# Performance work log

Measured on AMD Instinct MI355X. Metric: run time of the kernel, lower is better.

Reference implementation:

```python
import jax, jax.numpy as jnp
import numpy as np

B, T, C, HS = 16, 2048, 2048, 256  # batch, seq (=BLOCK_SIZE), N_EMBD, head_size


def setup_inputs() -> dict:
    key = jax.random.key(0)
    k0, k1, k2, k3 = jax.random.split(key, 4)
    token_embd = jax.random.normal(k0, (B, T, C), dtype=jnp.float32)
    # nn.Linear(C, HS, bias=False); store as [C, HS] so projection is x @ W
    scale = 1.0 / np.sqrt(C)
    Wk = jax.random.normal(k1, (C, HS), dtype=jnp.float32) * scale
    Wq = jax.random.normal(k2, (C, HS), dtype=jnp.float32) * scale
    Wv = jax.random.normal(k3, (C, HS), dtype=jnp.float32) * scale
    return {"token_embd": token_embd, "Wk": Wk, "Wq": Wq, "Wv": Wv}


def reference(token_embd, Wk, Wq, Wv):
    Bc, Tc, Cc = token_embd.shape
    k = token_embd @ Wk  # [B,T,HS]
    q = token_embd @ Wq  # [B,T,HS]
    v = token_embd @ Wv  # [B,T,HS]
    # NOTE faithful quirks of the source: k @ q^T (not q @ k^T) and
    # MULTIPLY by sqrt(C) where C = N_EMBD.
    weights = jnp.einsum("bih,bjh->bij", k, q) * (Cc ** 0.5)  # [B,T,T]
    # causal mask: tril==0 (upper triangle, j>i) -> -inf
    i = jnp.arange(Tc)[:, None]
    j = jnp.arange(Tc)[None, :]
    weights = jnp.where(j > i, -jnp.inf, weights)
    # softmax over dim=1 (rows / first T axis), as in the source
    weights = jax.nn.softmax(weights, axis=1)
    # dropout p=0.0 / eval mode -> identity
    output = jnp.einsum("bij,bjh->bih", weights, v)  # [B,T,HS]
    return output
```

## Files before the change

### kernel.cpp

```cpp
#include <hip/hip_runtime.h>
#include <math.h>

#define Bn 16
#define Tn 2048
#define Cn 2048
#define HSn 256
#define SCALE 45.254833995939045f
#define NEG_BIG (-1e30f)
#define NT 16
#define NPAIR 136
#define WN 524288

typedef __attribute__((ext_vector_type(8))) short bf16x8;
typedef __attribute__((ext_vector_type(4))) float f32x4;
typedef unsigned short u16;
typedef unsigned int u32;

__device__ __forceinline__ u16 bf16_rn(float f) {
    u32 u = __float_as_uint(f);
    u += 0x7fffu + ((u >> 16) & 1u);
    return (u16)(u >> 16);
}
__device__ __forceinline__ float bf16_rn_f(float f) {
    return __uint_as_float((u32)bf16_rn(f) << 16);
}

#define GLOAD_LDS16(gp, lp)                                                      \
    __builtin_amdgcn_global_load_lds(                                            \
        (const __attribute__((address_space(1))) unsigned int*)(gp),             \
        (__attribute__((address_space(3))) unsigned int*)(lp), 16, 0, 0)

#define WAITV0_LG0  asm volatile("s_waitcnt vmcnt(0) lgkmcnt(0)" ::: "memory")
#define WAITV2_LG0  asm volatile("s_waitcnt vmcnt(2) lgkmcnt(0)" ::: "memory")
#define WAITV32_LG0 asm volatile("s_waitcnt vmcnt(32) lgkmcnt(0)" ::: "memory")
#define WAITLG0     asm volatile("s_waitcnt lgkmcnt(0)" ::: "memory")
#define BARRIER     __builtin_amdgcn_s_barrier()

__global__ __launch_bounds__(256) void split_w_kernel(
    const float* __restrict__ Wk, const float* __restrict__ Wq,
    const float* __restrict__ Wv, u16* __restrict__ Wt)
{
    const int n = threadIdx.x, k = blockIdx.x, mat = blockIdx.y;
    const float* src = (mat == 0) ? Wk : (mat == 1) ? Wq : Wv;
    const float f = src[(long)k * HSn + n];
    const u32 u = __float_as_uint(f);
    const u16 hb = (u16)(u >> 16);
    const float fh = __uint_as_float(u & 0xffff0000u);
    const u16 lb = bf16_rn(f - fh);
    u16* base = Wt + (long)mat * 2 * WN;
    base[(long)n * Cn + k] = hb;
    base[WN + (long)n * Cn + k] = lb;
}

__global__ __launch_bounds__(512, 2) void projm_fused_kernel(
    const float* __restrict__ X, const u16* __restrict__ Wt,
    u16* __restrict__ Khi, u16* __restrict__ Klo,
    u16* __restrict__ Qhi, u16* __restrict__ Qlo, u16* __restrict__ VbfT)
{
    __shared__ u16 Ahi0[4096], Alo0[4096], Ahi1[4096], Alo1[4096];
    __shared__ u16 Bb0[20480], Bb1[20480];

    const int tid = threadIdx.x, l = tid & 63, w = tid >> 6;
    const int wm = w & 3, wn = w >> 2;
    const int m0 = blockIdx.x * 128, n0 = blockIdx.y * 128;

    int xoff[2], aoff[2];
    #pragma unroll
    for (int p = 0; p < 2; ++p) {
        const int idx4 = p * 512 + tid;
        const int row  = idx4 >> 3;
        const int kk4  = (idx4 & 7) * 4;
        xoff[p] = (m0 + row) * Cn + kk4;
        aoff[p] = (row >> 4) * 512 + (((row & 15) | ((kk4 >> 3) << 4)) * 8) + (kk4 & 7);
    }

    int wgoff[5];
    const int lbase = w * 5 * 512;
    #pragma unroll
    for (int j = 0; j < 5; ++j) {
        const int g    = w * 5 + j;
        const int half = g >> 3;
        const int cc   = g & 7;
        const int nrow = n0 + cc * 16 + (l & 15);
        wgoff[j] = half * WN + nrow * Cn + ((l >> 4) << 3);
    }

    f32x4 accK[2][4], accQ[2][4], accV[2][4];
    #pragma unroll
    for (int mt = 0; mt < 2; ++mt)
        #pragma unroll
        for (int nt = 0; nt < 4; ++nt)
            #pragma unroll
            for (int r = 0; r < 4; ++r) {
                accK[mt][nt][r] = 0.f; accQ[mt][nt][r] = 0.f; accV[mt][nt][r] = 0.f;
            }

    float4 xA[2], xB[2];

    auto convert_write = [&](const float4 (&xr)[2], u16* Ah, u16* Al) {
        #pragma unroll
        for (int p = 0; p < 2; ++p) {
            const float xf[4] = {xr[p].x, xr[p].y, xr[p].z, xr[p].w};
            ushort4 h4, l4;
            #pragma unroll
            for (int c = 0; c < 4; ++c) {
                const u32 u = __float_as_uint(xf[c]);
                ((u16*)&h4)[c] = (u16)(u >> 16);
                const float fh = __uint_as_float(u & 0xffff0000u);
                ((u16*)&l4)[c] = bf16_rn(xf[c] - fh);
            }
            *(ushort4*)(Ah + aoff[p]) = h4;
            *(ushort4*)(Al + aoff[p]) = l4;
        }
    };

    auto mfma_all = [&](const u16* Ah, const u16* Al, const u16* Bb) {
        bf16x8 ah[2], al[2];
        #pragma unroll
        for (int mt = 0; mt < 2; ++mt) {
            ah[mt] = *(const bf16x8*)(Ah + (wm * 2 + mt) * 512 + l * 8);
            al[mt] = *(const bf16x8*)(Al + (wm * 2 + mt) * 512 + l * 8);
        }
        {
            bf16x8 bh[4], bl[4];
            #pragma unroll
            for (int nt = 0; nt < 4; ++nt) {
                bh[nt] = *(const bf16x8*)(Bb + (0 * 8 + wn * 4 + nt) * 512 + l * 8);
                bl[nt] = *(const bf16x8*)(Bb + (1 * 8 + wn * 4 + nt) * 512 + l * 8);
            }
            #pragma unroll
            for (int mt = 0; mt < 2; ++mt)
                #pragma unroll
                for (int nt = 0; nt < 4; ++nt) {
                    accK[mt][nt] = __builtin_amdgcn_mfma_f32_16x16x32_bf16(ah[mt], bh[nt], accK[mt][nt], 0, 0, 0);
                    accK[mt][nt] = __builtin_amdgcn_mfma_f32_16x16x32_bf16(ah[mt], bl[nt], accK[mt][nt], 0, 0, 0);
                    accK[mt][nt] = __builtin_amdgcn_mfma_f32_16x16x32_bf16(al[mt], bh[nt], accK[mt][nt], 0, 0, 0);
                }
        }
        {
            bf16x8 bh[4], bl[4];
            #pragma unroll
            for (int nt = 0; nt < 4; ++nt) {
                bh[nt] = *(const bf16x8*)(Bb + (2 * 8 + wn * 4 + nt) * 512 + l * 8);
                bl[nt] = *(const bf16x8*)(Bb + (3 * 8 + wn * 4 + nt) * 512 + l * 8);
            }
            #pragma unroll
            for (int mt = 0; mt < 2; ++mt)
                #pragma unroll
                for (int nt = 0; nt < 4; ++nt) {
                    accQ[mt][nt] = __builtin_amdgcn_mfma_f32_16x16x32_bf16(ah[mt], bh[nt], accQ[mt][nt], 0, 0, 0);
                    accQ[mt][nt] = __builtin_amdgcn_mfma_f32_16x16x32_bf16(ah[mt], bl[nt], accQ[mt][nt], 0, 0, 0);
                    accQ[mt][nt] = __builtin_amdgcn_mfma_f32_16x16x32_bf16(al[mt], bh[nt], accQ[mt][nt], 0, 0, 0);
                }
        }
        {
            bf16x8 bh[4];
            #pragma unroll
            for (int nt = 0; nt < 4; ++nt)
                bh[nt] = *(const bf16x8*)(Bb + (4 * 8 + wn * 4 + nt) * 512 + l * 8);
            #pragma unroll
            for (int mt = 0; mt < 2; ++mt)
                #pragma unroll
                for (int nt = 0; nt < 4; ++nt)
                    accV[mt][nt] = __builtin_amdgcn_mfma_f32_16x16x32_bf16(ah[mt], bh[nt], accV[mt][nt], 0, 0, 0);
        }
    };

    xA[0] = *(const float4*)(X + xoff[0]);
    xA[1] = *(const float4*)(X + xoff[1]);
    #pragma unroll
    for (int j = 0; j < 5; ++j)
        GLOAD_LDS16(Wt + wgoff[j], Bb0 + lbase + j * 512);
    xB[0] = *(const float4*)(X + xoff[0] + 32);
    xB[1] = *(const float4*)(X + xoff[1] + 32);
    convert_write(xA, Ahi0, Alo0);
    WAITV2_LG0;
    BARRIER;

    #pragma unroll 1
    for (int k0 = 0; k0 < Cn; k0 += 64) {
        const int kn  = (k0 + 64 < Cn) ? k0 + 64 : 0;
        const int kn3 = (k0 + 96 < Cn) ? k0 + 96 : 0;
        #pragma unroll
        for (int j = 0; j < 5; ++j)
            GLOAD_LDS16(Wt + wgoff[j] + k0 + 32, Bb1 + lbase + j * 512);
        xA[0] = *(const float4*)(X + xoff[0] + kn);
        xA[1] = *(const float4*)(X + xoff[1] + kn);
        convert_write(xB, Ahi1, Alo1);
        mfma_all(Ahi0, Alo0, Bb0);
        WAITV2_LG0;
        BARRIER;
        #pragma unroll
        for (int j = 0; j < 5; ++j)
            GLOAD_LDS16(Wt + wgoff[j] + kn, Bb0 + lbase + j * 512);
        xB[0] = *(const float4*)(X + xoff[0] + kn3);
        xB[1] = *(const float4*)(X + xoff[1] + kn3);
        convert_write(xA, Ahi0, Alo0);
        mfma_all(Ahi1, Alo1, Bb1);
        WAITV2_LG0;
        BARRIER;
    }

    const int quad = (l >> 4) * 4, col = l & 15;
    u16* Vlds = Bb0;
    __syncthreads();
    #pragma unroll
    for (int mt = 0; mt < 2; ++mt)
        #pragma unroll
        for (int nt = 0; nt < 4; ++nt)
            #pragma unroll
            for (int r = 0; r < 4; ++r) {
                const long i = m0 + wm * 32 + mt * 16 + quad + r;
                const int  j = n0 + wn * 64 + nt * 16 + col;
                {
                    const float f = accK[mt][nt][r];
                    const u32 u = __float_as_uint(f);
                    Khi[i * HSn + j] = (u16)(u >> 16);
                    const float fh = __uint_as_float(u & 0xffff0000u);
                    Klo[i * HSn + j] = bf16_rn(f - fh);
                }
                {
                    const float f = accQ[mt][nt][r];
                    const u32 u = __float_as_uint(f);
                    Qhi[i * HSn + j] = (u16)(u >> 16);
                    const float fh = __uint_as_float(u & 0xffff0000u);
                    Qlo[i * HSn + j] = bf16_rn(f - fh);
                }
                Vlds[(wm * 32 + mt * 16 + quad + r) * 128 + wn * 64 + nt * 16 + col]
                    = bf16_rn(accV[mt][nt][r]);
            }
    __syncthreads();
    {
        const int bidx = m0 >> 11, jb = m0 & (Tn - 1);
        #pragma unroll
        for (int hh = 0; hh < 4; ++hh) {
            const int hl = hh * 32 + (tid >> 4);
            const int h  = n0 + hl;
            const int jl = (tid & 15) * 8;
            union { uint4 v; u16 s[8]; } pk;
            #pragma unroll
            for (int e = 0; e < 8; ++e) pk.s[e] = Vlds[(jl + e) * 128 + hl];
            *(uint4*)(VbfT + ((long)bidx * HSn + h) * Tn + jb + jl) = pk.v;
        }
    }
}

__device__ __forceinline__ void score_tile_mfma(
    const u16* __restrict__ Khi, const u16* __restrict__ Klo,
    const u16* __restrict__ Qhi, const u16* __restrict__ Qlo,
    long base, int i0, int j0,
    u16* Ab0, u16* Bb0,
    f32x4 (&acc)[4][4], int tid)
{
    const int l = tid & 63, w = tid >> 6;
    const int wm = w & 1, wn = w >> 1;
    const int lrow = l & 15, lk8 = (l >> 4) << 3;

    #pragma unroll
    for (int a = 0; a < 4; ++a)
        #pragma unroll
        for (int bb = 0; bb < 4; ++bb)
            #pragma unroll
            for (int r = 0; r < 4; ++r) acc[a][bb][r] = 0.f;

    const u16* hiP = wn ? Qhi : Khi;
    const u16* loP = wn ? Qlo : Klo;
    const int  t0  = wn ? j0 : i0;
    long rowoff[4];
    #pragma unroll
    for (int m2 = 0; m2 < 4; ++m2) {
        const int mt = (w & 1) * 4 + m2;
        rowoff[m2] = base + (long)(t0 + mt * 16 + lrow) * HSn + lk8;
    }
    u16* dst0 = (wn ? Bb0 : Ab0) + (w & 1) * 8 * 512;

    #pragma unroll 1
    for (int ks = 0; ks < 8; ++ks) {
        const int h0 = ks * 32;
        #pragma unroll
        for (int q = 0; q < 8; ++q) {
            const u16* sp = (q & 1) ? loP : hiP;
            GLOAD_LDS16(sp + rowoff[q >> 1] + h0, dst0 + q * 512);
        }
        WAITV0_LG0;
        BARRIER;
        bf16x8 bh[4], bl[4];
        #pragma unroll
        for (int nt = 0; nt < 4; ++nt) {
            const int c2 = (wn * 4 + nt) * 2;
            bh[nt] = *(const bf16x8*)(Bb0 + (c2    ) * 512 + l * 8);
            bl[nt] = *(const bf16x8*)(Bb0 + (c2 + 1) * 512 + l * 8);
        }
        #pragma unroll
        for (int mt = 0; mt < 4; ++mt) {
            const int c2 = (wm * 4 + mt) * 2;
            const bf16x8 ah = *(const bf16x8*)(Ab0 + (c2    ) * 512 + l * 8);
            const bf16x8 al = *(const bf16x8*)(Ab0 + (c2 + 1) * 512 + l * 8);
            #pragma unroll
            for (int nt = 0; nt < 4; ++nt) {
                acc[mt][nt] = __builtin_amdgcn_mfma_f32_16x16x32_bf16(ah, bh[nt], acc[mt][nt], 0, 0, 0);
                acc[mt][nt] = __builtin_amdgcn_mfma_f32_16x16x32_bf16(ah, bl[nt], acc[mt][nt], 0, 0, 0);
                acc[mt][nt] = __builtin_amdgcn_mfma_f32_16x16x32_bf16(al, bh[nt], acc[mt][nt], 0, 0, 0);
            }
        }
        WAITLG0;
        BARRIER;
    }
}

__device__ __forceinline__ void pair_from_p(int p, int& it, int& jt) {
    it = (int)((sqrtf(8.f * (float)p + 1.f) - 1.f) * 0.5f);
    while ((it + 1) * (it + 2) / 2 <= p) ++it;
    while (it * (it + 1) / 2 > p) --it;
    jt = p - it * (it + 1) / 2;
}

__global__ __launch_bounds__(256) void stats1_kernel(
    const u16* __restrict__ Khi, const u16* __restrict__ Klo,
    const u16* __restrict__ Qhi, const u16* __restrict__ Qlo,
    u16* __restrict__ Pm, u16* __restrict__ Pd)
{
    __shared__ u16 s_lds[16384];
    __shared__ float redm[2][128], redd[2][128];

    const int tid = threadIdx.x, l = tid & 63, w = tid >> 6;
    const int wm = w & 1, wn = w >> 1;
    const int b = blockIdx.y;
    int it, jt; pair_from_p(blockIdx.x, it, jt);
    const long base = (long)b * Tn * HSn;

    f32x4 acc[4][4];
    score_tile_mfma(Khi, Klo, Qhi, Qlo, base, it * 128, jt * 128,
                    s_lds, s_lds + 8192, acc, tid);

    const int rquad = (l >> 4) * 4, col = l & 15;
    #pragma unroll
    for (int nt = 0; nt < 4; ++nt) {
        const int j = jt * 128 + wn * 64 + nt * 16 + col;
        float m = NEG_BIG;
        #pragma unroll
        for (int mt = 0; mt < 4; ++mt)
            #pragma unroll
            for (int r = 0; r < 4; ++r) {
                const int i = it * 128 + wm * 64 + mt * 16 + rquad + r;
                const float sv = (i >= j) ? acc[mt][nt][r] * SCALE : NEG_BIG;
                acc[mt][nt][r] = sv;
                m = fmaxf(m, sv);
            }
        m = fmaxf(m, __shfl_xor(m, 16));
        m = fmaxf(m, __shfl_xor(m, 32));
        float d = 0.f;
        #pragma unroll
        for (int mt = 0; mt < 4; ++mt)
            #pragma unroll
            for (int r = 0; r < 4; ++r)
                d += __expf(acc[mt][nt][r] - m);
        d += __shfl_xor(d, 16);
        d += __shfl_xor(d, 32);
        if (l < 16) {
            redm[wm][wn * 64 + nt * 16 + l] = m;
            redd[wm][wn * 64 + nt * 16 + l] = d;
        }
    }
    __syncthreads();
    if (tid < 128) {
        const float m0 = redm[0][tid], m1 = redm[1][tid];
        const float d0 = redd[0][tid], d1 = redd[1][tid];
        const float M = fmaxf(m0, m1);
        float D = d0 * __expf(m0 - M) + d1 * __expf(m1 - M);
        const float Mb = bf16_rn_f(M);
        D *= __expf(M - Mb);
        const long idx = ((long)b * NPAIR + blockIdx.x) * 128 + tid;
        Pm[idx] = (u16)(__float_as_uint(Mb) >> 16);
        Pd[idx] = bf16_rn(D);
    }
}

__global__ __launch_bounds__(128) void stats2_kernel(
    const u16* __restrict__ Pm, const u16* __restrict__ Pd,
    float* __restrict__ Ms, float* __restrict__ Rd)
{
    const int b = blockIdx.y, jt = blockIdx.x, jl = threadIdx.x;
    float M = NEG_BIG, D = 0.f;
    for (int it = jt; it < NT; ++it) {
        const int p = it * (it + 1) / 2 + jt;
        const long idx = ((long)b * NPAIR + p) * 128 + jl;
        const float m = __uint_as_float((u32)Pm[idx] << 16);
        const float d = __uint_as_float((u32)Pd[idx] << 16);
        const float Mn = fmaxf(M, m);
        D = D * __expf(M - Mn) + d * __expf(m - Mn);
        M = Mn;
    }
    Ms[(long)b * Tn + jt * 128 + jl] = M;
    Rd[(long)b * Tn + jt * 128 + jl] = 1.f / D;
}

__global__ __launch_bounds__(256) void out_kernel(
    const u16* __restrict__ Khi, const u16* __restrict__ Klo,
    const u16* __restrict__ Qhi, const u16* __restrict__ Qlo,
    const u16* __restrict__ VbfT, const float* __restrict__ Ms,
    const float* __restrict__ Rd, float* __restrict__ Out)
{
    __shared__ u16 u_lds[25600];
    u16* Pf    = u_lds;
    u16* Vfrag = u_lds + 17408;

    const int tid = threadIdx.x, l = tid & 63, w = tid >> 6;
    const int wm = w & 1, wn = w >> 1;
    const int lrow = l & 15, lk8 = (l >> 4) << 3;
    const int b = blockIdx.y;
    int it, jt; pair_from_p(blockIdx.x, it, jt);
    const long base = (long)b * Tn * HSn;

    f32x4 acc[4][4];
    score_tile_mfma(Khi, Klo, Qhi, Qlo, base, it * 128, jt * 128,
                    u_lds, u_lds + 8192, acc, tid);

    auto stage_v = [&](int ph) {
        #pragma unroll
        for (int q = 0; q < 4; ++q) {
            const int hh = ph * 64 + q * 16 + lrow;
            const long ga = ((long)b * HSn + hh) * Tn + jt * 128 + w * 32 + lk8;
            GLOAD_LDS16(VbfT + ga, Vfrag + (w * 4 + q) * 512);
        }
    };

    stage_v(0);

    const int rquad = (l >> 4) * 4, col = l & 15;
    float mj[4], rj[4];
    #pragma unroll
    for (int nt = 0; nt < 4; ++nt) {
        const int j = jt * 128 + wn * 64 + nt * 16 + col;
        mj[nt] = Ms[(long)b * Tn + j];
        rj[nt] = Rd[(long)b * Tn + j];
    }
    #pragma unroll
    for (int nt = 0; nt < 4; ++nt) {
        const int j = jt * 128 + wn * 64 + nt * 16 + col;
        #pragma unroll
        for (int mt = 0; mt < 4; ++mt)
            #pragma unroll
            for (int r = 0; r < 4; ++r) {
                const int i = it * 128 + wm * 64 + mt * 16 + rquad + r;
                const float pv = (i >= j)
                    ? __expf(acc[mt][nt][r] * SCALE - mj[nt]) * rj[nt] : 0.f;
                Pf[(wm * 64 + mt * 16 + rquad + r) * 136 + wn * 64 + nt * 16 + col]
                    = bf16_rn(pv);
            }
    }

    __syncthreads();

    #pragma unroll 1
    for (int ph = 0; ph < 4; ++ph) {
        f32x4 o[4][2];
        #pragma unroll
        for (int a = 0; a < 4; ++a)
            #pragma unroll
            for (int bb = 0; bb < 2; ++bb)
                #pragma unroll
                for (int r = 0; r < 4; ++r) o[a][bb][r] = 0.f;
        #pragma unroll
        for (int kj = 0; kj < 4; ++kj) {
            bf16x8 aP[4];
            #pragma unroll
            for (int mt = 0; mt < 4; ++mt)
                aP[mt] = *(const bf16x8*)(Pf + (wm * 64 + mt * 16 + lrow) * 136 + kj * 32 + lk8);
            #pragma unroll
            for (int nt = 0; nt < 2; ++nt) {
                const bf16x8 bV = *(const bf16x8*)(Vfrag + (kj * 4 + wn * 2 + nt) * 512 + l * 8);
                #pragma unroll
                for (int mt = 0; mt < 4; ++mt)
                    o[mt][nt] = __builtin_amdgcn_mfma_f32_16x16x32_bf16(aP[mt], bV, o[mt][nt], 0, 0, 0);
            }
        }
        WAITLG0;
        BARRIER;
        if (ph < 3) stage_v(ph + 1);
        __builtin_amdgcn_sched_barrier(0);
        #pragma unroll
        for (int mt = 0; mt < 4; ++mt)
            #pragma unroll
            for (int nt = 0; nt < 2; ++nt)
                #pragma unroll
                for (int r = 0; r < 4; ++r) {
                    const int i = it * 128 + wm * 64 + mt * 16 + rquad + r;
                    const int h = ph * 64 + wn * 32 + nt * 16 + col;
                    atomicAdd(&Out[((long)b * Tn + i) * HSn + h], o[mt][nt][r]);
                }
        if (ph < 3) {
            WAITV32_LG0;
            BARRIER;
        }
    }
}

extern "C" void kernel_launch(void* const* d_in, const int* in_sizes, int n_in,
                              void* d_out, int out_size, void* d_ws, size_t ws_size,
                              hipStream_t stream) {
    const float* X  = (const float*)d_in[0];
    const float* Wk = (const float*)d_in[1];
    const float* Wq = (const float*)d_in[2];
    const float* Wv = (const float*)d_in[3];

    const long nE = (long)Bn * Tn * HSn;
    u16* Khi = (u16*)d_ws;
    u16* Klo = Khi + nE;
    u16* Qhi = Khi + 2 * nE;
    u16* Qlo = Khi + 3 * nE;
    u16* VbfT = Khi + 4 * nE;
    u16* Wt  = Khi + 5 * nE;
    u16* Pm  = Wt + 6L * WN;
    u16* Pd  = Pm + (long)Bn * NPAIR * 128;
    float* Ms = (float*)(Pd + (long)Bn * NPAIR * 128);
    float* Rd = Ms + (long)Bn * Tn;

    split_w_kernel<<<dim3(Cn, 3), 256, 0, stream>>>(Wk, Wq, Wv, Wt);
    projm_fused_kernel<<<dim3((Bn * Tn) / 128, HSn / 128), 512, 0, stream>>>(
        X, Wt, Khi, Klo, Qhi, Qlo, VbfT);
    stats1_kernel<<<dim3(NPAIR, Bn), 256, 0, stream>>>(Khi, Klo, Qhi, Qlo, Pm, Pd);
    stats2_kernel<<<dim3(NT, Bn), 128, 0, stream>>>(Pm, Pd, Ms, Rd);
    hipMemsetAsync(d_out, 0, (size_t)out_size * sizeof(float), stream);
    out_kernel<<<dim3(NPAIR, Bn), 256, 0, stream>>>(Khi, Klo, Qhi, Qlo, VbfT, Ms, Rd,
                                                    (float*)d_out);
}
```

Before: 975.4 us.

## Store weights, K/Q hi-lo and V in MFMA fragment-tiled layouts

Weights, K/Q hi/lo splits and V are now written in pre-swizzled 512-element fragment blocks that match the LDS layout the MFMA loaders expect. Each global_load_lds then reads one contiguous 1 KB chunk per wave instead of strided row segments. The V transpose through LDS at the end of the projection kernel, along with its two syncthreads, is removed. The cost is scattered 2-byte stores in the projection epilogue and in split_w, and a workspace layout every consumer now depends on.

```diff
diff --git a/kernel.cpp b/kernel.cpp
--- a/kernel.cpp
+++ b/kernel.cpp
@@ -36,9 +36,10 @@
 #define WAITLG0     asm volatile("s_waitcnt lgkmcnt(0)" ::: "memory")
 #define BARRIER     __builtin_amdgcn_s_barrier()
 
+
 __global__ __launch_bounds__(256) void split_w_kernel(
     const float* __restrict__ Wk, const float* __restrict__ Wq,
-    const float* __restrict__ Wv, u16* __restrict__ Wt)
+    const float* __restrict__ Wv, u16* __restrict__ Wf)
 {
     const int n = threadIdx.x, k = blockIdx.x, mat = blockIdx.y;
     const float* src = (mat == 0) ? Wk : (mat == 1) ? Wq : Wv;
@@ -47,15 +48,19 @@
     const u16 hb = (u16)(u >> 16);
     const float fh = __uint_as_float(u & 0xffff0000u);
     const u16 lb = bf16_rn(f - fh);
-    u16* base = Wt + (long)mat * 2 * WN;
-    base[(long)n * Cn + k] = hb;
-    base[WN + (long)n * Cn + k] = lb;
+
+    const int ntile = n >> 7, cc = (n >> 4) & 7, lrow = n & 15;
+    const int kst = k >> 5, kk = k & 31;
+    const int pos = ((((kk >> 3) << 4) | lrow) * 8) + (kk & 7);
+    const long c0 = (((long)(mat * 2 + 0) * 2 + ntile) * 64 + kst) * 8 + cc;
+    const long c1 = c0 + 2 * 64 * 8;
+    Wf[c0 * 512 + pos] = hb;
+    Wf[c1 * 512 + pos] = lb;
 }
 
 __global__ __launch_bounds__(512, 2) void projm_fused_kernel(
-    const float* __restrict__ X, const u16* __restrict__ Wt,
-    u16* __restrict__ Khi, u16* __restrict__ Klo,
-    u16* __restrict__ Qhi, u16* __restrict__ Qlo, u16* __restrict__ VbfT)
+    const float* __restrict__ X, const u16* __restrict__ Wf,
+    u16* __restrict__ Kf, u16* __restrict__ Qf, u16* __restrict__ Vf)
 {
     __shared__ u16 Ahi0[4096], Alo0[4096], Ahi1[4096], Alo1[4096];
     __shared__ u16 Bb0[20480], Bb1[20480];
@@ -81,8 +86,7 @@
         const int g    = w * 5 + j;
         const int half = g >> 3;
         const int cc   = g & 7;
-        const int nrow = n0 + cc * 16 + (l & 15);
-        wgoff[j] = half * WN + nrow * Cn + ((l >> 4) << 3);
+        wgoff[j] = (half * 2 + (n0 >> 7)) * 262144 + cc * 512 + l * 8;
     }
 
     f32x4 accK[2][4], accQ[2][4], accV[2][4];
@@ -170,7 +174,7 @@
     xA[1] = *(const float4*)(X + xoff[1]);
     #pragma unroll
     for (int j = 0; j < 5; ++j)
-        GLOAD_LDS16(Wt + wgoff[j], Bb0 + lbase + j * 512);
+        GLOAD_LDS16(Wf + wgoff[j], Bb0 + lbase + j * 512);
     xB[0] = *(const float4*)(X + xoff[0] + 32);
     xB[1] = *(const float4*)(X + xoff[1] + 32);
     convert_write(xA, Ahi0, Alo0);
@@ -183,7 +187,7 @@
         const int kn3 = (k0 + 96 < Cn) ? k0 + 96 : 0;
         #pragma unroll
         for (int j = 0; j < 5; ++j)
-            GLOAD_LDS16(Wt + wgoff[j] + k0 + 32, Bb1 + lbase + j * 512);
+            GLOAD_LDS16(Wf + wgoff[j] + ((k0 + 32) >> 5) * 4096, Bb1 + lbase + j * 512);
         xA[0] = *(const float4*)(X + xoff[0] + kn);
         xA[1] = *(const float4*)(X + xoff[1] + kn);
         convert_write(xB, Ahi1, Alo1);
@@ -192,7 +196,7 @@
         BARRIER;
         #pragma unroll
         for (int j = 0; j < 5; ++j)
-            GLOAD_LDS16(Wt + wgoff[j] + kn, Bb0 + lbase + j * 512);
+            GLOAD_LDS16(Wf + wgoff[j] + (kn >> 5) * 4096, Bb0 + lbase + j * 512);
         xB[0] = *(const float4*)(X + xoff[0] + kn3);
         xB[1] = *(const float4*)(X + xoff[1] + kn3);
         convert_write(xA, Ahi0, Alo0);
@@ -202,59 +206,50 @@
     }
 
     const int quad = (l >> 4) * 4, col = l & 15;
-    u16* Vlds = Bb0;
-    __syncthreads();
+    const int bidx = m0 >> 11, tile = (m0 >> 7) & 15;
+    const long kqbase = (long)(bidx * 16 + tile) * 128 * 512;
+    const long vbase  = (long)(bidx * 16 + tile) * 64 * 512;
     #pragma unroll
     for (int mt = 0; mt < 2; ++mt)
         #pragma unroll
         for (int nt = 0; nt < 4; ++nt)
             #pragma unroll
             for (int r = 0; r < 4; ++r) {
-                const long i = m0 + wm * 32 + mt * 16 + quad + r;
-                const int  j = n0 + wn * 64 + nt * 16 + col;
+                const int lrow = quad + r;
+                const int mt8  = wm * 2 + mt;
+                const int ks   = (n0 >> 5) + wn * 2 + (nt >> 1);
+                const int hpos = ((((nt & 1) * 2 + (col >> 3)) * 16 + lrow) * 8) + (col & 7);
+                const long kqoff = kqbase + (long)(ks * 16 + mt8 * 2) * 512 + hpos;
                 {
                     const float f = accK[mt][nt][r];
                     const u32 u = __float_as_uint(f);
-                    Khi[i * HSn + j] = (u16)(u >> 16);
+                    Kf[kqoff]       = (u16)(u >> 16);
                     const float fh = __uint_as_float(u & 0xffff0000u);
-                    Klo[i * HSn + j] = bf16_rn(f - fh);
+                    Kf[kqoff + 512] = bf16_rn(f - fh);
                 }
                 {
                     const float f = accQ[mt][nt][r];
                     const u32 u = __float_as_uint(f);
-                    Qhi[i * HSn + j] = (u16)(u >> 16);
+                    Qf[kqoff]       = (u16)(u >> 16);
                     const float fh = __uint_as_float(u & 0xffff0000u);
-                    Qlo[i * HSn + j] = bf16_rn(f - fh);
+                    Qf[kqoff + 512] = bf16_rn(f - fh);
                 }
-                Vlds[(wm * 32 + mt * 16 + quad + r) * 128 + wn * 64 + nt * 16 + col]
-                    = bf16_rn(accV[mt][nt][r]);
-            }
-    __syncthreads();
-    {
-        const int bidx = m0 >> 11, jb = m0 & (Tn - 1);
-        #pragma unroll
-        for (int hh = 0; hh < 4; ++hh) {
-            const int hl = hh * 32 + (tid >> 4);
-            const int h  = n0 + hl;
-            const int jl = (tid & 15) * 8;
-            union { uint4 v; u16 s[8]; } pk;
-            #pragma unroll
-            for (int e = 0; e < 8; ++e) pk.s[e] = Vlds[(jl + e) * 128 + hl];
-            *(uint4*)(VbfT + ((long)bidx * HSn + h) * Tn + jb + jl) = pk.v;
-        }
-    }
+                {
+                    const int hg   = (n0 >> 4) + wn * 4 + nt;
+                    const int posv = ((col | ((mt * 2 + (lrow >> 3)) << 4)) * 8) + (lrow & 7);
+                    Vf[vbase + (long)(wm * 16 + hg) * 512 + posv] = bf16_rn(accV[mt][nt][r]);
+                }
+            }
 }
 
 __device__ __forceinline__ void score_tile_mfma(
-    const u16* __restrict__ Khi, const u16* __restrict__ Klo,
-    const u16* __restrict__ Qhi, const u16* __restrict__ Qlo,
-    long base, int i0, int j0,
+    const u16* __restrict__ Kf, const u16* __restrict__ Qf,
+    int b, int it, int jt,
     u16* Ab0, u16* Bb0,
     f32x4 (&acc)[4][4], int tid)
 {
     const int l = tid & 63, w = tid >> 6;
     const int wm = w & 1, wn = w >> 1;
-    const int lrow = l & 15, lk8 = (l >> 4) << 3;
 
     #pragma unroll
     for (int a = 0; a < 4; ++a)
@@ -263,25 +258,17 @@
             #pragma unroll
             for (int r = 0; r < 4; ++r) acc[a][bb][r] = 0.f;
 
-    const u16* hiP = wn ? Qhi : Khi;
-    const u16* loP = wn ? Qlo : Klo;
-    const int  t0  = wn ? j0 : i0;
-    long rowoff[4];
-    #pragma unroll
-    for (int m2 = 0; m2 < 4; ++m2) {
-        const int mt = (w & 1) * 4 + m2;
-        rowoff[m2] = base + (long)(t0 + mt * 16 + lrow) * HSn + lk8;
-    }
+    const u16* srcP = wn ? Qf : Kf;
+    const long tbase = (long)(b * 16 + (wn ? jt : it)) * 128 * 512
+                     + (w & 1) * 8 * 512 + l * 8;
     u16* dst0 = (wn ? Bb0 : Ab0) + (w & 1) * 8 * 512;
 
     #pragma unroll 1
     for (int ks = 0; ks < 8; ++ks) {
-        const int h0 = ks * 32;
-        #pragma unroll
-        for (int q = 0; q < 8; ++q) {
-            const u16* sp = (q & 1) ? loP : hiP;
-            GLOAD_LDS16(sp + rowoff[q >> 1] + h0, dst0 + q * 512);
-        }
+        const long sb = tbase + (long)ks * 16 * 512;
+        #pragma unroll
+        for (int q = 0; q < 8; ++q)
+            GLOAD_LDS16(srcP + sb + q * 512, dst0 + q * 512);
         WAITV0_LG0;
         BARRIER;
         bf16x8 bh[4], bl[4];
@@ -316,8 +303,7 @@
 }
 
 __global__ __launch_bounds__(256) void stats1_kernel(
-    const u16* __restrict__ Khi, const u16* __restrict__ Klo,
-    const u16* __restrict__ Qhi, const u16* __restrict__ Qlo,
+    const u16* __restrict__ Kf, const u16* __restrict__ Qf,
     u16* __restrict__ Pm, u16* __restrict__ Pd)
 {
     __shared__ u16 s_lds[16384];
@@ -327,11 +313,9 @@
     const int wm = w & 1, wn = w >> 1;
     const int b = blockIdx.y;
     int it, jt; pair_from_p(blockIdx.x, it, jt);
-    const long base = (long)b * Tn * HSn;
 
     f32x4 acc[4][4];
-    score_tile_mfma(Khi, Klo, Qhi, Qlo, base, it * 128, jt * 128,
-                    s_lds, s_lds + 8192, acc, tid);
+    score_tile_mfma(Kf, Qf, b, it, jt, s_lds, s_lds + 8192, acc, tid);
 
     const int rquad = (l >> 4) * 4, col = l & 15;
     #pragma unroll
@@ -396,9 +380,8 @@
 }
 
 __global__ __launch_bounds__(256) void out_kernel(
-    const u16* __restrict__ Khi, const u16* __restrict__ Klo,
-    const u16* __restrict__ Qhi, const u16* __restrict__ Qlo,
-    const u16* __restrict__ VbfT, const float* __restrict__ Ms,
+    const u16* __restrict__ Kf, const u16* __restrict__ Qf,
+    const u16* __restrict__ Vf, const float* __restrict__ Ms,
     const float* __restrict__ Rd, float* __restrict__ Out)
 {
     __shared__ u16 u_lds[25600];
@@ -410,19 +393,15 @@
     const int lrow = l & 15, lk8 = (l >> 4) << 3;
     const int b = blockIdx.y;
     int it, jt; pair_from_p(blockIdx.x, it, jt);
-    const long base = (long)b * Tn * HSn;
 
     f32x4 acc[4][4];
-    score_tile_mfma(Khi, Klo, Qhi, Qlo, base, it * 128, jt * 128,
-                    u_lds, u_lds + 8192, acc, tid);
-
+    score_tile_mfma(Kf, Qf, b, it, jt, u_lds, u_lds + 8192, acc, tid);
+
+    const long vb = (long)(b * 16 + jt) * 64 * 512 + (long)w * 16 * 512 + l * 8;
     auto stage_v = [&](int ph) {
         #pragma unroll
-        for (int q = 0; q < 4; ++q) {
-            const int hh = ph * 64 + q * 16 + lrow;
-            const long ga = ((long)b * HSn + hh) * Tn + jt * 128 + w * 32 + lk8;
-            GLOAD_LDS16(VbfT + ga, Vfrag + (w * 4 + q) * 512);
-        }
+        for (int q = 0; q < 4; ++q)
+            GLOAD_LDS16(Vf + vb + (ph * 4 + q) * 512, Vfrag + (w * 4 + q) * 512);
     };
 
     stage_v(0);
@@ -505,23 +484,21 @@
     const float* Wv = (const float*)d_in[3];
 
     const long nE = (long)Bn * Tn * HSn;
-    u16* Khi = (u16*)d_ws;
-    u16* Klo = Khi + nE;
-    u16* Qhi = Khi + 2 * nE;
-    u16* Qlo = Khi + 3 * nE;
-    u16* VbfT = Khi + 4 * nE;
-    u16* Wt  = Khi + 5 * nE;
-    u16* Pm  = Wt + 6L * WN;
-    u16* Pd  = Pm + (long)Bn * NPAIR * 128;
+    u16* Kf = (u16*)d_ws;
+    u16* Qf = Kf + 2 * nE;
+    u16* Vf = Kf + 4 * nE;
+    u16* Wf = Kf + 5 * nE;
+    u16* Pm = Wf + 6L * WN;
+    u16* Pd = Pm + (long)Bn * NPAIR * 128;
     float* Ms = (float*)(Pd + (long)Bn * NPAIR * 128);
     float* Rd = Ms + (long)Bn * Tn;
 
-    split_w_kernel<<<dim3(Cn, 3), 256, 0, stream>>>(Wk, Wq, Wv, Wt);
+    split_w_kernel<<<dim3(Cn, 3), 256, 0, stream>>>(Wk, Wq, Wv, Wf);
     projm_fused_kernel<<<dim3((Bn * Tn) / 128, HSn / 128), 512, 0, stream>>>(
-        X, Wt, Khi, Klo, Qhi, Qlo, VbfT);
-    stats1_kernel<<<dim3(NPAIR, Bn), 256, 0, stream>>>(Khi, Klo, Qhi, Qlo, Pm, Pd);
+        X, Wf, Kf, Qf, Vf);
+    stats1_kernel<<<dim3(NPAIR, Bn), 256, 0, stream>>>(Kf, Qf, Pm, Pd);
     stats2_kernel<<<dim3(NT, Bn), 128, 0, stream>>>(Pm, Pd, Ms, Rd);
     hipMemsetAsync(d_out, 0, (size_t)out_size * sizeof(float), stream);
-    out_kernel<<<dim3(NPAIR, Bn), 256, 0, stream>>>(Khi, Klo, Qhi, Qlo, VbfT, Ms, Rd,
+    out_kernel<<<dim3(NPAIR, Bn), 256, 0, stream>>>(Kf, Qf, Vf, Ms, Rd,
                                                     (float*)d_out);
 }
```

Result: faster. 930.6 us (-4.6%).
